# Optimization experiments

Hardware: AMD Instinct MI355X
Metric: run time of the kernel (lower is better)

The kernel has to match this reference:

```python
import jax
jax.config.update("jax_enable_x64", True)
import jax.numpy as jnp
from jax import lax
import numpy as np

SR, LOWER, UPPER, ORDER = 16000, 500, 7000, 8


def _butter_bandpass_ba(N, lower, upper, sr):
    """Replicates scipy.signal.butter(N, [2*lo/sr, 2*hi/sr], 'bandpass')."""
    Wn = np.array([2.0 * lower / sr, 2.0 * upper / sr])
    fs = 2.0
    warped = 2.0 * fs * np.tan(np.pi * Wn / fs)  # pre-warp for bilinear
    # analog Butterworth lowpass prototype (buttap)
    m = np.arange(-N + 1, N, 2)
    p = -np.exp(1j * np.pi * m / (2 * N))
    k = 1.0
    # lp2bp_zpk
    bw = warped[1] - warped[0]
    wo = np.sqrt(warped[0] * warped[1])
    degree = len(p)  # no finite zeros in prototype
    p_lp = p * bw / 2.0
    p_bp = np.concatenate([p_lp + np.sqrt(p_lp ** 2 - wo ** 2),
                           p_lp - np.sqrt(p_lp ** 2 - wo ** 2)])
    z_bp = np.zeros(degree, dtype=complex)
    k_bp = k * bw ** degree
    # bilinear_zpk (fs=2)
    fs2 = 2.0 * fs
    z_d = (fs2 + z_bp) / (fs2 - z_bp)
    p_d = (fs2 + p_bp) / (fs2 - p_bp)
    z_d = np.append(z_d, -np.ones(len(p_bp) - len(z_bp)))
    k_d = k_bp * np.real(np.prod(fs2 - z_bp) / np.prod(fs2 - p_bp))
    b = np.real(k_d * np.poly(z_d))
    a = np.real(np.poly(p_d))
    return b, a


def _lfilter_zi(b, a):
    """Replicates scipy.signal.lfilter_zi (steady-state of step response)."""
    n = len(a)
    comp = np.zeros((n - 1, n - 1))
    comp[0, :] = -a[1:] / a[0]
    comp[1:, :-1] = np.eye(n - 2)
    IminusA = np.eye(n - 1) - comp.T
    B = b[1:] - a[1:] * b[0]
    return np.linalg.solve(IminusA, B)


def _lfilter(b, a, x, zi):
    """Direct-form II transposed IIR filter. x: [B, L], zi: [B, n-1]."""
    b0, bt, at = b[0], b[1:], a[1:]

    def step(z, xt):  # z: [B, n-1], xt: [B]
        y = b0 * xt + z[:, 0]
        z_shift = jnp.concatenate([z[:, 1:], jnp.zeros_like(z[:, :1])], axis=1)
        z_new = z_shift + xt[:, None] * bt[None, :] - y[:, None] * at[None, :]
        return z_new, y

    _, y = lax.scan(step, zi, x.T)
    return y.T


def _filtfilt(b, a, x):
    """Replicates scipy.signal.filtfilt defaults (padtype='odd', method='pad')."""
    padlen = 3 * max(len(a), len(b))
    # odd extension along time
    left = 2.0 * x[:, :1] - x[:, 1:padlen + 1][:, ::-1]
    right = 2.0 * x[:, -1:] - x[:, -padlen - 1:-1][:, ::-1]
    ext = jnp.concatenate([left, x, right], axis=1)
    zi = jnp.asarray(_lfilter_zi(b, a))[None, :]  # [1, n-1]
    bj, aj = jnp.asarray(b), jnp.asarray(a)
    y = _lfilter(bj, aj, ext, zi * ext[:, :1])          # forward pass
    yr = y[:, ::-1]
    y = _lfilter(bj, aj, yr, zi * yr[:, :1])            # backward pass
    y = y[:, ::-1]
    return y[:, padlen:-padlen]


def setup_inputs() -> dict:
    key = jax.random.key(0)
    audio = jax.random.normal(key, (32, 262144), dtype=jnp.float32)
    return {"audio": audio}


def reference(audio) -> jnp.ndarray:
    b, a = _butter_bandpass_ba(ORDER, LOWER, UPPER, SR)
    y = _filtfilt(b, a, audio.astype(jnp.float64))
    return y.astype(jnp.float32)
```

## Files before the change

### kernel.cpp

```cpp
#include <hip/hip_runtime.h>
#include <cmath>
#include <complex>

#define NB    32
#define LX    262144
#define PAD   51
#define LTOT  (LX + 2 * PAD)
#define CM    32
#define F_PAD 1946
#define LPAD  (LTOT + F_PAD)
#define CPB   64
#define TILE  (CPB * CM)
#define NTILE (LPAD / TILE)
#define NP    8
#define LDSR  34
#define WIN   16

struct CoeffsS { float a1[NP], a2[NP], b0[NP], b1[NP], c0; };
struct LvS { float lv[6][NP][4]; };

__global__ void k_init(float4* __restrict__ mt, LvS L) {
    int id = blockIdx.x * 256 + threadIdx.x;
    if (id >= 512) return;
    int t = id >> 3, q = id & 7;
    float m0 = 1.f, m1 = 0.f, m2 = 0.f, m3 = 1.f;
    for (int k = 0; k < 6; k++)
        if ((t >> k) & 1) {
            float a0 = L.lv[k][q][0], a1 = L.lv[k][q][1];
            float a2 = L.lv[k][q][2], a3 = L.lv[k][q][3];
            float n0 = a0 * m0 + a1 * m2, n1 = a0 * m1 + a1 * m3;
            float n2 = a2 * m0 + a3 * m2, n3 = a2 * m1 + a3 * m3;
            m0 = n0; m1 = n1; m2 = n2; m3 = n3;
        }
    mt[id] = make_float4(m0, m1, m2, m3);
}

__device__ __forceinline__ void load_uA(const float* __restrict__ x,
                                        float base, int c, float (&u)[CM]) {
    int t0 = c * CM - F_PAD;
    if (t0 >= PAD && t0 + CM <= PAD + LX) {
        const float* xs = x + (t0 - PAD);
#pragma unroll
        for (int m = 0; m < CM / 4; m++) {
            float4 v = *reinterpret_cast<const float4*>(xs + 4 * m);
            u[4 * m] = v.x - base; u[4 * m + 1] = v.y - base;
            u[4 * m + 2] = v.z - base; u[4 * m + 3] = v.w - base;
        }
    } else {
#pragma unroll
        for (int i = 0; i < CM; i++) {
            int t = t0 + i;
            float uu;
            if (t < 0) uu = 0.f;
            else {
                float e;
                if (t < PAD)            e = 2.0f * x[0] - x[PAD - t];
                else if (t < PAD + LX)  e = x[t - PAD];
                else                    e = 2.0f * x[LX - 1] - x[2 * LX + PAD - 2 - t];
                uu = e - base;
            }
            u[i] = uu;
        }
    }
}

__device__ __forceinline__ void load_uB(const float* __restrict__ yb,
                                        float base, int c, float (&u)[CM]) {
    if (c < 0) {
#pragma unroll
        for (int i = 0; i < CM; i++) u[i] = 0.f;
        return;
    }
    const float* ys = yb + (size_t)c * CM;
#pragma unroll
    for (int m = 0; m < CM / 4; m++) {
        float4 v = *reinterpret_cast<const float4*>(ys + 4 * m);
        u[4 * m] = v.x - base; u[4 * m + 1] = v.y - base;
        u[4 * m + 2] = v.z - base; u[4 * m + 3] = v.w - base;
    }
}

__device__ __forceinline__ void local_states(const float (&u)[CM], const CoeffsS& C,
                                             float (&w1)[NP], float (&w2)[NP]) {
#pragma unroll
    for (int q = 0; q < NP; q++) { w1[q] = 0.f; w2[q] = 0.f; }
#pragma unroll
    for (int i = 0; i < CM; i++) {
        float uu = u[i];
#pragma unroll
        for (int q = 0; q < NP; q++) {
            float wt = fmaf(C.a1[q], w1[q], fmaf(C.a2[q], w2[q], uu));
            w2[q] = w1[q]; w1[q] = wt;
        }
    }
}

__device__ __forceinline__ void pack_states(float4* sc4, int j,
                                            const float (&w1)[NP], const float (&w2)[NP]) {
#pragma unroll
    for (int p = 0; p < 4; p++)
        sc4[p * 80 + j] = make_float4(w1[2 * p], w2[2 * p], w1[2 * p + 1], w2[2 * p + 1]);
}

template <int PASS>
__global__ __launch_bounds__(64) void k_full(const float* __restrict__ in,
                                             float* __restrict__ outp,
                                             const float4* __restrict__ mt,
                                             CoeffsS C) {
    __shared__ __align__(16) float lds[CPB * LDSR];
    float4* sc4 = reinterpret_cast<float4*>(lds);
    int tid = threadIdx.x, tx = blockIdx.x, b = blockIdx.y;
    int c = tx * CPB + tid;

    const float* x = in + (size_t)b * (PASS == 0 ? LX : LPAD);
    float base = (PASS == 0) ? (2.0f * x[0] - x[PAD]) : x[0];

    if (tid < WIN) {
        float uw[CM];
        int cw = tx * CPB - WIN + tid;
        if (PASS == 0) load_uA(x, base, cw, uw);
        else           load_uB(x, base, cw, uw);
        float w1[NP], w2[NP];
        local_states(uw, C, w1, w2);
        pack_states(sc4, tid, w1, w2);
    }

    float u[CM];
    if (PASS == 0) load_uA(x, base, c, u);
    else           load_uB(x, base, c, u);
    float w1[NP], w2[NP];
    local_states(u, C, w1, w2);
    pack_states(sc4, WIN + tid, w1, w2);
    __syncthreads();

    float e1[NP], e2[NP];
#pragma unroll
    for (int q = 0; q < NP; q++) { e1[q] = 0.f; e2[q] = 0.f; }
#pragma unroll
    for (int k = 1; k <= WIN; k++) {
#pragma unroll
        for (int p = 0; p < 4; p++) {
            float4 f = sc4[p * 80 + WIN + tid - k];
            float4 ma = mt[(k - 1) * NP + 2 * p];
            float4 mb = mt[(k - 1) * NP + 2 * p + 1];
            e1[2 * p]     = fmaf(ma.x, f.x, fmaf(ma.y, f.y, e1[2 * p]));
            e2[2 * p]     = fmaf(ma.z, f.x, fmaf(ma.w, f.y, e2[2 * p]));
            e1[2 * p + 1] = fmaf(mb.x, f.z, fmaf(mb.y, f.w, e1[2 * p + 1]));
            e2[2 * p + 1] = fmaf(mb.z, f.z, fmaf(mb.w, f.w, e2[2 * p + 1]));
        }
    }

#pragma unroll
    for (int q = 0; q < NP; q++) { w1[q] = e1[q]; w2[q] = e2[q]; }
#pragma unroll
    for (int i = 0; i < CM; i++) {
        float uu = u[i];
        float y = C.c0 * uu;
#pragma unroll
        for (int q = 0; q < NP; q++) {
            float wt = fmaf(C.a1[q], w1[q], fmaf(C.a2[q], w2[q], uu));
            y = fmaf(C.b0[q], wt, fmaf(C.b1[q], w1[q], y));
            w2[q] = w1[q]; w1[q] = wt;
        }
        u[i] = y;
    }

    __syncthreads();
    if (PASS == 0) {
#pragma unroll
        for (int k = 0; k < CM / 2; k++)
            *reinterpret_cast<float2*>(&lds[tid * LDSR + 2 * k]) =
                make_float2(u[2 * k], u[2 * k + 1]);
    } else {
#pragma unroll
        for (int i = 0; i < CM; i++) lds[tid * LDSR + i] = u[i];
    }
    __syncthreads();

    if (PASS == 0) {
        float4* yb4 = reinterpret_cast<float4*>(
            outp + (size_t)b * LPAD + (size_t)(NTILE - 1 - tx) * TILE);
#pragma unroll
        for (int k = 0; k < 8; k++) {
            int o4 = tid + 64 * k;
            int ts = 63 - (o4 >> 3);
            int ih = 31 - 4 * (o4 & 7);
            float2 a  = *reinterpret_cast<const float2*>(&lds[ts * LDSR + ih - 1]);
            float2 b2 = *reinterpret_cast<const float2*>(&lds[ts * LDSR + ih - 3]);
            yb4[o4] = make_float4(a.y, a.x, b2.y, b2.x);
        }
    } else {
        float* ob = outp + (size_t)b * LX;
        int J0 = (LTOT - 1 - PAD) - tx * TILE;
#pragma unroll
        for (int it = 0; it < CM; it++) {
            int o = it * 64 + tid;
            int j = J0 - o;
            if (j >= 0 && j < LX)
                ob[j] = lds[(o >> 5) * LDSR + (o & 31)];
        }
    }
}

static void compute_coeffs(CoeffsS& C, LvS& L) {
    using cd = std::complex<double>;
    const int N = 8;
    const double sr = 16000.0, lo = 500.0, hi = 7000.0, fs = 2.0;
    double w0 = 2.0 * fs * std::tan(M_PI * (2.0 * lo / sr) / fs);
    double w1 = 2.0 * fs * std::tan(M_PI * (2.0 * hi / sr) / fs);
    double bw = w1 - w0, wo = std::sqrt(w0 * w1);
    cd pbp[16];
    for (int k = 0; k < N; k++) {
        int m = -N + 1 + 2 * k;
        cd pl = -std::exp(cd(0.0, M_PI * m / (2.0 * N)));
        pl *= bw / 2.0;
        cd s = std::sqrt(pl * pl - cd(wo * wo, 0.0));
        pbp[k] = pl + s; pbp[k + N] = pl - s;
    }
    double kbp = std::pow(bw, (double)N);
    const double fs2 = 4.0;
    cd pd[16], denom = 1.0;
    for (int i = 0; i < 16; i++) {
        pd[i] = (cd(fs2, 0.0) + pbp[i]) / (cd(fs2, 0.0) - pbp[i]);
        denom *= (cd(fs2, 0.0) - pbp[i]);
    }
    double kd = kbp * std::real(cd(std::pow(fs2, 8.0), 0.0) / denom);
    cd prodp = 1.0;
    for (int i = 0; i < 16; i++) prodp *= pd[i];
    cd c0 = cd(kd, 0.0) / prodp;
    int n = 0;
    for (int i = 0; i < 16; i++) {
        if (pd[i].imag() <= 0.0) continue;
        cd inv = 1.0 / pd[i];
        cd t1 = cd(1.0, 0.0) - inv, t2 = cd(1.0, 0.0) + inv;
        cd numr = cd(kd, 0.0);
        for (int k = 0; k < 8; k++) numr *= t1;
        for (int k = 0; k < 8; k++) numr *= t2;
        cd den = 1.0;
        for (int j = 0; j < 16; j++)
            if (j != i) den *= (cd(1.0, 0.0) - pd[j] * inv);
        cd r2 = 2.0 * numr / den;
        if (n < NP) {
            double a1 = 2.0 * pd[i].real();
            double a2 = -std::norm(pd[i]);
            C.a1[n] = (float)a1; C.a2[n] = (float)a2;
            C.b0[n] = (float)r2.real();
            C.b1[n] = (float)(-(r2.real() * pd[i].real() + r2.imag() * pd[i].imag()));
            double M[4] = { a1, a2, 1.0, 0.0 };
            for (int s = 0; s < 5; s++) {
                double q0 = M[0] * M[0] + M[1] * M[2], q1 = M[0] * M[1] + M[1] * M[3];
                double q2 = M[2] * M[0] + M[3] * M[2], q3 = M[2] * M[1] + M[3] * M[3];
                M[0] = q0; M[1] = q1; M[2] = q2; M[3] = q3;
            }
            for (int k = 0; k < 6; k++) {
                for (int j = 0; j < 4; j++) L.lv[k][n][j] = (float)M[j];
                double q0 = M[0] * M[0] + M[1] * M[2], q1 = M[0] * M[1] + M[1] * M[3];
                double q2 = M[2] * M[0] + M[3] * M[2], q3 = M[2] * M[1] + M[3] * M[3];
                M[0] = q0; M[1] = q1; M[2] = q2; M[3] = q3;
            }
            n++;
        }
    }
    C.c0 = (float)c0.real();
}

extern "C" void kernel_launch(void* const* d_in, const int* in_sizes, int n_in,
                              void* d_out, int out_size, void* d_ws, size_t ws_size,
                              hipStream_t stream) {
    const float* audio = (const float*)d_in[0];
    float* out = (float*)d_out;

    CoeffsS C; LvS L;
    compute_coeffs(C, L);

    char* ws = (char*)d_ws;
    size_t o = 0;
    auto alloc = [&](size_t bytes) { size_t r = o; o += (bytes + 255) & ~(size_t)255; return r; };
    float*  ybuf = (float*)(ws + alloc((size_t)NB * LPAD * sizeof(float)));
    float4* mt   = (float4*)(ws + alloc(512 * sizeof(float4)));

    dim3 blkw(64), g(NTILE, NB);

    k_init   <<<2, 256, 0, stream>>>(mt, L);
    k_full<0><<<g, blkw, 0, stream>>>(audio, ybuf, mt, C);
    k_full<1><<<g, blkw, 0, stream>>>(ybuf, out, mt, C);
}
```

Baseline: 72.40 us.

## Halve per-thread chunk length and pack two wavefronts per block

Reduces the samples each thread processes serially from 32 to 16, which doubles the number of independent chunks and threads and shortens each thread's serial recurrence. Each block now holds two independent 64-lane wavefronts, each with its own LDS region, and the matrix-power table is rebuilt for 16-sample strides. The change aims to expose more parallelism and latency hiding for the IIR scan. In exchange, the window-propagation overhead per output sample roughly doubles, and the LDS readback for the reversed output now uses scalar reads instead of float2 reads.

Result: faster. 66.71 us (-7.9%).

```diff
diff --git a/kernel.cpp b/kernel.cpp
--- a/kernel.cpp
+++ b/kernel.cpp
@@ -6,15 +6,16 @@
 #define LX    262144
 #define PAD   51
 #define LTOT  (LX + 2 * PAD)
-#define CM    32
+#define CM    16
 #define F_PAD 1946
 #define LPAD  (LTOT + F_PAD)
-#define CPB   64
-#define TILE  (CPB * CM)
+#define TILE  (64 * CM)
 #define NTILE (LPAD / TILE)
+#define WPB   2
 #define NP    8
-#define LDSR  34
+#define LDSR  17
 #define WIN   16
+#define WREG  1280
 
 struct CoeffsS { float a1[NP], a2[NP], b0[NP], b1[NP], c0; };
 struct LvS { float lv[6][NP][4]; };
@@ -103,26 +104,28 @@
 }
 
 template <int PASS>
-__global__ __launch_bounds__(64) void k_full(const float* __restrict__ in,
-                                             float* __restrict__ outp,
-                                             const float4* __restrict__ mt,
-                                             CoeffsS C) {
-    __shared__ __align__(16) float lds[CPB * LDSR];
-    float4* sc4 = reinterpret_cast<float4*>(lds);
-    int tid = threadIdx.x, tx = blockIdx.x, b = blockIdx.y;
-    int c = tx * CPB + tid;
+__global__ __launch_bounds__(128) void k_full(const float* __restrict__ in,
+                                              float* __restrict__ outp,
+                                              const float4* __restrict__ mt,
+                                              CoeffsS C) {
+    __shared__ __align__(16) float lds[WPB * WREG];
+    int tid = threadIdx.x, wv = tid >> 6, l = tid & 63;
+    int ttx = blockIdx.x * WPB + wv, b = blockIdx.y;
+    int c = ttx * 64 + l;
+    float* wlds = lds + wv * WREG;
+    float4* sc4 = reinterpret_cast<float4*>(wlds);
 
     const float* x = in + (size_t)b * (PASS == 0 ? LX : LPAD);
     float base = (PASS == 0) ? (2.0f * x[0] - x[PAD]) : x[0];
 
-    if (tid < WIN) {
+    if (l < WIN) {
         float uw[CM];
-        int cw = tx * CPB - WIN + tid;
+        int cw = ttx * 64 - WIN + l;
         if (PASS == 0) load_uA(x, base, cw, uw);
         else           load_uB(x, base, cw, uw);
         float w1[NP], w2[NP];
         local_states(uw, C, w1, w2);
-        pack_states(sc4, tid, w1, w2);
+        pack_states(sc4, l, w1, w2);
     }
 
     float u[CM];
@@ -130,7 +133,7 @@
     else           load_uB(x, base, c, u);
     float w1[NP], w2[NP];
     local_states(u, C, w1, w2);
-    pack_states(sc4, WIN + tid, w1, w2);
+    pack_states(sc4, WIN + l, w1, w2);
     __syncthreads();
 
     float e1[NP], e2[NP];
@@ -140,7 +143,7 @@
     for (int k = 1; k <= WIN; k++) {
 #pragma unroll
         for (int p = 0; p < 4; p++) {
-            float4 f = sc4[p * 80 + WIN + tid - k];
+            float4 f = sc4[p * 80 + WIN + l - k];
             float4 ma = mt[(k - 1) * NP + 2 * p];
             float4 mb = mt[(k - 1) * NP + 2 * p + 1];
             e1[2 * p]     = fmaf(ma.x, f.x, fmaf(ma.y, f.y, e1[2 * p]));
@@ -166,38 +169,30 @@
     }
 
     __syncthreads();
-    if (PASS == 0) {
-#pragma unroll
-        for (int k = 0; k < CM / 2; k++)
-            *reinterpret_cast<float2*>(&lds[tid * LDSR + 2 * k]) =
-                make_float2(u[2 * k], u[2 * k + 1]);
-    } else {
-#pragma unroll
-        for (int i = 0; i < CM; i++) lds[tid * LDSR + i] = u[i];
-    }
+#pragma unroll
+    for (int i = 0; i < CM; i++) wlds[l * LDSR + i] = u[i];
     __syncthreads();
 
     if (PASS == 0) {
         float4* yb4 = reinterpret_cast<float4*>(
-            outp + (size_t)b * LPAD + (size_t)(NTILE - 1 - tx) * TILE);
-#pragma unroll
-        for (int k = 0; k < 8; k++) {
-            int o4 = tid + 64 * k;
-            int ts = 63 - (o4 >> 3);
-            int ih = 31 - 4 * (o4 & 7);
-            float2 a  = *reinterpret_cast<const float2*>(&lds[ts * LDSR + ih - 1]);
-            float2 b2 = *reinterpret_cast<const float2*>(&lds[ts * LDSR + ih - 3]);
-            yb4[o4] = make_float4(a.y, a.x, b2.y, b2.x);
+            outp + (size_t)b * LPAD + (size_t)(NTILE - 1 - ttx) * TILE);
+#pragma unroll
+        for (int k = 0; k < 4; k++) {
+            int o4 = l + 64 * k;
+            int ts = 63 - (o4 >> 2);
+            int ih = 15 - 4 * (o4 & 3);
+            const float* r = &wlds[ts * LDSR];
+            yb4[o4] = make_float4(r[ih], r[ih - 1], r[ih - 2], r[ih - 3]);
         }
     } else {
         float* ob = outp + (size_t)b * LX;
-        int J0 = (LTOT - 1 - PAD) - tx * TILE;
+        int J0 = (LTOT - 1 - PAD) - ttx * TILE;
 #pragma unroll
         for (int it = 0; it < CM; it++) {
-            int o = it * 64 + tid;
+            int o = it * 64 + l;
             int j = J0 - o;
             if (j >= 0 && j < LX)
-                ob[j] = lds[(o >> 5) * LDSR + (o & 31)];
+                ob[j] = wlds[(o >> 4) * LDSR + (o & 15)];
         }
     }
 }
@@ -247,7 +242,7 @@
             C.b0[n] = (float)r2.real();
             C.b1[n] = (float)(-(r2.real() * pd[i].real() + r2.imag() * pd[i].imag()));
             double M[4] = { a1, a2, 1.0, 0.0 };
-            for (int s = 0; s < 5; s++) {
+            for (int s = 0; s < 4; s++) {
                 double q0 = M[0] * M[0] + M[1] * M[2], q1 = M[0] * M[1] + M[1] * M[3];
                 double q2 = M[2] * M[0] + M[3] * M[2], q3 = M[2] * M[1] + M[3] * M[3];
                 M[0] = q0; M[1] = q1; M[2] = q2; M[3] = q3;
@@ -279,9 +274,9 @@
     float*  ybuf = (float*)(ws + alloc((size_t)NB * LPAD * sizeof(float)));
     float4* mt   = (float4*)(ws + alloc(512 * sizeof(float4)));
 
-    dim3 blkw(64), g(NTILE, NB);
+    dim3 blk(128), g(NTILE / WPB, NB);
 
     k_init   <<<2, 256, 0, stream>>>(mt, L);
-    k_full<0><<<g, blkw, 0, stream>>>(audio, ybuf, mt, C);
-    k_full<1><<<g, blkw, 0, stream>>>(ybuf, out, mt, C);
-}
+    k_full<0><<<g, blk, 0, stream>>>(audio, ybuf, mt, C);
+    k_full<1><<<g, blk, 0, stream>>>(ybuf, out, mt, C);
+}
```
